# Performance work log

Hardware: AMD Instinct MI355X
Metric: run time of the kernel (lower is better)

## Reference

```python
import jax, jax.numpy as jnp
import numpy as np
from jax import lax

B, T, D = 2048, 300, 40
H = 64          # BasicLSTMCell num_units
D1 = 128        # dense1 units
OUT = 512       # out_dim (num speakers)
FORGET_BIAS = 1.0
BN_EPS = 1e-3   # tf.layers.BatchNormalization default


def setup_inputs() -> dict:
    key = jax.random.key(0)
    ks = jax.random.split(key, 10)
    X = jax.random.normal(ks[0], (B, T, D), dtype=jnp.float32)
    seq_length = jax.random.randint(ks[1], (B,), 1, T + 1).astype(jnp.int32)
    # BasicLSTMCell kernel: [input_dim + H, 4H], gate order i, j, f, o
    lstm_kernel = jax.random.normal(ks[2], (D + H, 4 * H), dtype=jnp.float32) * 0.08
    lstm_bias = jnp.zeros((4 * H,), dtype=jnp.float32)
    W1 = jax.random.normal(ks[3], (H, D1), dtype=jnp.float32) * 0.1
    b1 = jnp.zeros((D1,), dtype=jnp.float32)
    gamma = jnp.ones((D1,), dtype=jnp.float32)
    beta = jnp.zeros((D1,), dtype=jnp.float32)
    moving_mean = jnp.zeros((D1,), dtype=jnp.float32)
    moving_var = jnp.ones((D1,), dtype=jnp.float32)
    W2 = jax.random.normal(ks[4], (D1, OUT), dtype=jnp.float32) * 0.1
    b2 = jnp.zeros((OUT,), dtype=jnp.float32)
    return {"X": X, "seq_length": seq_length,
            "lstm_kernel": lstm_kernel, "lstm_bias": lstm_bias,
            "W1": W1, "b1": b1, "gamma": gamma, "beta": beta,
            "moving_mean": moving_mean, "moving_var": moving_var,
            "W2": W2, "b2": b2}


def reference(X, seq_length, lstm_kernel, lstm_bias, W1, b1, gamma, beta,
              moving_mean, moving_var, W2, b2):
    b = X.shape[0]
    c0 = jnp.zeros((b, H), dtype=X.dtype)
    h0 = jnp.zeros((b, H), dtype=X.dtype)

    def step(carry, x_t):
        c, h = carry
        z = jnp.concatenate([x_t, h], axis=1) @ lstm_kernel + lstm_bias
        i, j, f, o = jnp.split(z, 4, axis=1)
        new_c = c * jax.nn.sigmoid(f + FORGET_BIAS) + jax.nn.sigmoid(i) * jnp.tanh(j)
        new_h = jnp.tanh(new_c) * jax.nn.sigmoid(o)
        return (new_c, new_h), new_h

    _, outs = lax.scan(step, (c0, h0), jnp.swapaxes(X, 0, 1))  # [T, B, H]
    outs = jnp.swapaxes(outs, 0, 1)  # [B, T, H]

    # gather last valid timestep per sample
    idx = (seq_length - 1).astype(jnp.int32)
    final = jnp.take_along_axis(outs, idx[:, None, None], axis=1)[:, 0, :]  # [B, H]

    x = jax.nn.relu(final @ W1 + b1)
    # BatchNorm in inference mode (training=False): use moving statistics
    x = gamma * (x - moving_mean) * lax.rsqrt(moving_var + BN_EPS) + beta
    return jax.nn.softmax(x @ W2 + b2, axis=-1)
```

## Files before the change

kernel.cpp:

```cpp
#include <hip/hip_runtime.h>
#include <stdint.h>

#define TT 300
#define DD 40
#define SB 8
#define AROWH 192
#define ABYTES (16 * AROWH * 2)
#define WROW 224

typedef __attribute__((ext_vector_type(8))) short short8;
typedef __attribute__((ext_vector_type(4))) float f32x4;

__device__ __forceinline__ ushort f2bf(float f) {
  uint32_t b = __float_as_uint(f);
  b += 0x7FFFu + ((b >> 16) & 1u);
  return (ushort)(b >> 16);
}

__device__ __forceinline__ void bar() {
  asm volatile("s_waitcnt lgkmcnt(0)" ::: "memory");
  __builtin_amdgcn_s_barrier();
  asm volatile("" ::: "memory");
}

__device__ __forceinline__ int aswz(int row, int colh) {
  return ((row * AROWH + colh) * 2) ^ ((row & 7) << 4);
}

__global__ __launch_bounds__(512, 2) void lstm_mfma_kernel(
    const float* __restrict__ X, const int* __restrict__ seqlen,
    const float* __restrict__ Wk, const float* __restrict__ bias,
    float* __restrict__ hfin)
{
  __shared__ ushort shmem[64 * WROW];
  char* const Ab = reinterpret_cast<char*>(shmem);

  const int tid = threadIdx.x;
  const int wv = tid >> 6, lane = tid & 63;
  const int q = lane >> 4, n = lane & 15, m = n & 7, b = n >> 3;
  const int s0 = blockIdx.x * SB;

  short8 Bf[6][2];
  for (int c = 0; c < 4; ++c) {
    for (int i = tid; i < 64 * 192; i += 512) {
      int cc = i & 63, kp = i >> 6;
      int nb = cc & 15, nt = (cc >> 4) & 1, ws = cc >> 5;
      int g = nt + 2 * (nb >> 3);
      int uu = (2 * c + ws) * 8 + (nb & 7);
      int col = g * 64 + uu;
      ushort v = 0;
      if (kp < 40) {
        v = f2bf(Wk[kp * 256 + col]);
      } else if (kp < 42) {
        float bv = bias[col] + ((g == 2) ? 1.0f : 0.0f);
        ushort hi = f2bf(bv);
        v = (kp == 40) ? hi : f2bf(bv - __uint_as_float((uint32_t)hi << 16));
      } else if (kp >= 64) {
        v = f2bf(Wk[(40 + ((kp - 64) >> 1)) * 256 + col]);
      }
      shmem[cc * WROW + kp] = v;
    }
    __syncthreads();
    if ((wv >> 1) == c) {
      const int cbase = (wv & 1) * 32;
      #pragma unroll
      for (int kt = 0; kt < 6; ++kt) {
        #pragma unroll
        for (int nt = 0; nt < 2; ++nt)
          Bf[kt][nt] = *reinterpret_cast<const short8*>(
              &shmem[(cbase + nt * 16 + n) * WROW + kt * 32 + q * 8]);
      }
    }
    __syncthreads();
  }

  for (int i = tid; i < 6144; i += 512) shmem[i] = 0;
  __syncthreads();

  const int u = wv * 8 + m;
  const int sl = 2 * q + b;
  const int len = seqlen[s0 + sl];
  int ml = seqlen[s0 + (lane & 7)];
  #pragma unroll
  for (int off = 1; off < 8; off <<= 1) ml = max(ml, __shfl_xor(ml, off));

  const bool hasX = (tid < SB * DD);
  const int sA = (tid * 205) >> 13, dA = tid - sA * 40;
  const int rA = 4 * (sA >> 1) + (sA & 1);
  const float* pA = X + (size_t)(s0 + sA) * (TT * DD) + dA;
  const int xb = aswz(rA, dA);

  if (tid < 16) {
    int s = tid & 7, bb = tid >> 3;
    int row = 4 * (s >> 1) + (s & 1);
    *reinterpret_cast<uint32_t*>(Ab + bb * ABYTES + aswz(row, 40)) = 0x3F803F80u;
  }
  float xv = 0.f;
  if (hasX) {
    *reinterpret_cast<ushort*>(Ab + xb) = f2bf(pA[0]);
    if (ml > 1) xv = pA[DD];
  }
  __syncthreads();
  pA += 2 * DD;

  int aoff[6];
  #pragma unroll
  for (int kt = 0; kt < 6; ++kt)
    aoff[kt] = (n * 384 + kt * 64 + q * 16) ^ (m << 4);

  float cst = 0.f, hf = 0.f;
  int rb = 0, wb = ABYTES;
  const int hb = aswz(4 * q + b, 64 + 2 * u);

  for (int t = 0; t < ml; ++t) {
    short8 Ax0 = *reinterpret_cast<const short8*>(Ab + rb + aoff[0]);
    short8 Ax1 = *reinterpret_cast<const short8*>(Ab + rb + aoff[1]);
    short8 Ah[4];
    #pragma unroll
    for (int k2 = 0; k2 < 4; ++k2)
      Ah[k2] = *reinterpret_cast<const short8*>(Ab + rb + aoff[k2 + 2]);

    f32x4 zero4 = {0.f, 0.f, 0.f, 0.f};
    f32x4 ac0[2], ac1[2], ac2[2], ac3[2];
    #pragma unroll
    for (int nt = 0; nt < 2; ++nt) {
      ac0[nt] = __builtin_amdgcn_mfma_f32_16x16x32_bf16(Ax0, Bf[0][nt], zero4, 0, 0, 0);
      ac0[nt] = __builtin_amdgcn_mfma_f32_16x16x32_bf16(Ax1, Bf[1][nt], ac0[nt], 0, 0, 0);
    }

    if (hasX && t + 1 < ml) *reinterpret_cast<ushort*>(Ab + wb + xb) = f2bf(xv);
    float xn = 0.f;
    if (hasX && t + 2 < ml) { xn = pA[0]; pA += DD; }

    #pragma unroll
    for (int nt = 0; nt < 2; ++nt) {
      ac1[nt] = __builtin_amdgcn_mfma_f32_16x16x32_bf16(Ah[0], Bf[2][nt], zero4, 0, 0, 0);
      ac2[nt] = __builtin_amdgcn_mfma_f32_16x16x32_bf16(Ah[1], Bf[3][nt], zero4, 0, 0, 0);
      ac3[nt] = __builtin_amdgcn_mfma_f32_16x16x32_bf16(Ah[2], Bf[4][nt], zero4, 0, 0, 0);
      ac0[nt] = __builtin_amdgcn_mfma_f32_16x16x32_bf16(Ah[3], Bf[5][nt], ac0[nt], 0, 0, 0);
    }
    f32x4 z0 = (ac0[0] + ac1[0]) + (ac2[0] + ac3[0]);
    f32x4 z1 = (ac0[1] + ac1[1]) + (ac2[1] + ac3[1]);

    float p00 = __shfl_xor(z0[0], 8);
    float p01 = __shfl_xor(z0[1], 8);
    float p10 = __shfl_xor(z1[0], 8);
    float p11 = __shfl_xor(z1[1], 8);
    float gi = b ? p01 : z0[0];
    float gf = b ? z0[1] : p00;
    float gj = b ? p11 : z1[0];
    float go = b ? z1[1] : p10;

    float Ef = __expf(-gf), Ei = __expf(-gi), Ej = __expf(2.f * gj);
    float nc = fmaf(cst, __builtin_amdgcn_rcpf(1.f + Ef),
                    (Ej - 1.f) * __builtin_amdgcn_rcpf((1.f + Ei) * (1.f + Ej)));
    float En = __expf(2.f * fminf(nc, 44.f)), Eo = __expf(-go);
    float nh = (En - 1.f) * __builtin_amdgcn_rcpf((1.f + En) * (1.f + Eo));
    cst = nc;
    if (t == len - 1) hf = nh;

    ushort hh = (ushort)(__float_as_uint(nh) >> 16);
    float rem = nh - __uint_as_float((uint32_t)hh << 16);
    ushort hl = (ushort)(__float_as_uint(rem) >> 16);
    *reinterpret_cast<uint32_t*>(Ab + wb + hb) = (uint32_t)hh | ((uint32_t)hl << 16);

    bar();
    rb ^= ABYTES; wb ^= ABYTES;
    xv = xn;
  }

  hfin[(size_t)(s0 + sl) * 64 + u] = hf;
}

__global__ __launch_bounds__(256, 1) void head_kernel(
    const float* __restrict__ hfin,
    const float* __restrict__ W1, const float* __restrict__ b1,
    const float* __restrict__ gamma, const float* __restrict__ beta,
    const float* __restrict__ mmean, const float* __restrict__ mvar,
    const float* __restrict__ W2, const float* __restrict__ b2,
    float* __restrict__ out)
{
  __shared__ float hl[16 * 64];
  __shared__ float d1t[128 * 20];
  __shared__ float lg[16 * 516];
  const int tid = threadIdx.x;
  const int b0 = blockIdx.x * 16;

  for (int i = tid; i < 16 * 64; i += 256) hl[i] = hfin[(size_t)b0 * 64 + i];
  __syncthreads();

  {
    const int j = tid & 127, sg = tid >> 7;
    float acc[8];
    const float bb = b1[j];
    #pragma unroll
    for (int s = 0; s < 8; ++s) acc[s] = bb;
    for (int k = 0; k < 64; ++k) {
      float w = W1[k * 128 + j];
      #pragma unroll
      for (int s = 0; s < 8; ++s) acc[s] = fmaf(hl[(sg * 8 + s) * 64 + k], w, acc[s]);
    }
    const float ga = gamma[j], be = beta[j], mm = mmean[j];
    const float iv = rsqrtf(mvar[j] + 1e-3f);
    #pragma unroll
    for (int s = 0; s < 8; ++s) {
      float v = fmaxf(acc[s], 0.f);
      d1t[j * 20 + sg * 8 + s] = ga * (v - mm) * iv + be;
    }
  }
  __syncthreads();

  {
    const int cA = tid * 2;
    float accA[16], accB[16];
    const float bA = b2[cA], bB = b2[cA + 1];
    #pragma unroll
    for (int s = 0; s < 16; ++s) { accA[s] = bA; accB[s] = bB; }
    for (int k = 0; k < 128; ++k) {
      const float2 w = *reinterpret_cast<const float2*>(&W2[k * 512 + cA]);
      const f32x4 dq0 = *reinterpret_cast<const f32x4*>(&d1t[k * 20]);
      const f32x4 dq1 = *reinterpret_cast<const f32x4*>(&d1t[k * 20 + 4]);
      const f32x4 dq2 = *reinterpret_cast<const f32x4*>(&d1t[k * 20 + 8]);
      const f32x4 dq3 = *reinterpret_cast<const f32x4*>(&d1t[k * 20 + 12]);
      #pragma unroll
      for (int s = 0; s < 4; ++s) {
        accA[s]      = fmaf(dq0[s], w.x, accA[s]);      accB[s]      = fmaf(dq0[s], w.y, accB[s]);
        accA[s + 4]  = fmaf(dq1[s], w.x, accA[s + 4]);  accB[s + 4]  = fmaf(dq1[s], w.y, accB[s + 4]);
        accA[s + 8]  = fmaf(dq2[s], w.x, accA[s + 8]);  accB[s + 8]  = fmaf(dq2[s], w.y, accB[s + 8]);
        accA[s + 12] = fmaf(dq3[s], w.x, accA[s + 12]); accB[s + 12] = fmaf(dq3[s], w.y, accB[s + 12]);
      }
    }
    #pragma unroll
    for (int s = 0; s < 16; ++s) {
      lg[s * 516 + cA]     = accA[s];
      lg[s * 516 + cA + 1] = accB[s];
    }
  }
  __syncthreads();

  {
    const int w = tid >> 6, lane = tid & 63;
    #pragma unroll
    for (int si = 0; si < 4; ++si) {
      const int s = w * 4 + si;
      float v[8];
      float mx = -3.4e38f;
      #pragma unroll
      for (int i = 0; i < 8; ++i) { v[i] = lg[s * 516 + lane + 64 * i]; mx = fmaxf(mx, v[i]); }
      #pragma unroll
      for (int off = 1; off < 64; off <<= 1) mx = fmaxf(mx, __shfl_xor(mx, off));
      float sum = 0.f;
      #pragma unroll
      for (int i = 0; i < 8; ++i) { v[i] = __expf(v[i] - mx); sum += v[i]; }
      #pragma unroll
      for (int off = 1; off < 64; off <<= 1) sum += __shfl_xor(sum, off);
      const float inv = __builtin_amdgcn_rcpf(sum);
      #pragma unroll
      for (int i = 0; i < 8; ++i)
        out[(size_t)(b0 + s) * 512 + lane + 64 * i] = v[i] * inv;
    }
  }
}

extern "C" void kernel_launch(void* const* d_in, const int* in_sizes, int n_in,
                              void* d_out, int out_size, void* d_ws, size_t ws_size,
                              hipStream_t stream) {
  const float* X      = (const float*)d_in[0];
  const int*   seqlen = (const int*)d_in[1];
  const float* Wk     = (const float*)d_in[2];
  const float* bias   = (const float*)d_in[3];
  const float* W1     = (const float*)d_in[4];
  const float* b1     = (const float*)d_in[5];
  const float* gam    = (const float*)d_in[6];
  const float* bet    = (const float*)d_in[7];
  const float* mmean  = (const float*)d_in[8];
  const float* mvar   = (const float*)d_in[9];
  const float* W2     = (const float*)d_in[10];
  const float* b2     = (const float*)d_in[11];
  float* out  = (float*)d_out;
  float* hfin = (float*)d_ws;

  lstm_mfma_kernel<<<dim3(2048 / SB), dim3(512), 0, stream>>>(X, seqlen, Wk, bias, hfin);
  head_kernel<<<dim3(128), dim3(256), 0, stream>>>(hfin, W1, b1, gam, bet,
                                                   mmean, mvar, W2, b2, out);
}
```

Baseline: 363.5 us.

## Compact A tile to 8 rows, single accumulator chain, unroll double buffer

Result: faster. 350.7 us (-3.5%).

```diff
diff --git a/kernel.cpp b/kernel.cpp
--- a/kernel.cpp
+++ b/kernel.cpp
@@ -4,8 +4,7 @@
 #define TT 300
 #define DD 40
 #define SB 8
-#define AROWH 192
-#define ABYTES (16 * AROWH * 2)
+#define ABYTES (8 * 192 * 2)
 #define WROW 224
 
 typedef __attribute__((ext_vector_type(8))) short short8;
@@ -24,7 +23,7 @@
 }
 
 __device__ __forceinline__ int aswz(int row, int colh) {
-  return ((row * AROWH + colh) * 2) ^ ((row & 7) << 4);
+  return ((row * 192 + colh) * 2) ^ (row << 4);
 }
 
 __global__ __launch_bounds__(512, 2) void lstm_mfma_kernel(
@@ -74,11 +73,12 @@
     __syncthreads();
   }
 
-  for (int i = tid; i < 6144; i += 512) shmem[i] = 0;
-  __syncthreads();
-
+  for (int i = tid; i < 3072; i += 512) shmem[i] = 0;
+  __syncthreads();
+
+  const int hi2 = q >> 1;
   const int u = wv * 8 + m;
-  const int sl = 2 * q + b;
+  const int sl = (q & 1) * 4 + hi2 * 2 + b;
   const int len = seqlen[s0 + sl];
   int ml = seqlen[s0 + (lane & 7)];
   #pragma unroll
@@ -86,14 +86,12 @@
 
   const bool hasX = (tid < SB * DD);
   const int sA = (tid * 205) >> 13, dA = tid - sA * 40;
-  const int rA = 4 * (sA >> 1) + (sA & 1);
   const float* pA = X + (size_t)(s0 + sA) * (TT * DD) + dA;
-  const int xb = aswz(rA, dA);
+  const int xb = aswz(sA, dA);
 
   if (tid < 16) {
     int s = tid & 7, bb = tid >> 3;
-    int row = 4 * (s >> 1) + (s & 1);
-    *reinterpret_cast<uint32_t*>(Ab + bb * ABYTES + aswz(row, 40)) = 0x3F803F80u;
+    *reinterpret_cast<uint32_t*>(Ab + bb * ABYTES + aswz(s, 40)) = 0x3F803F80u;
   }
   float xv = 0.f;
   if (hasX) {
@@ -106,50 +104,53 @@
   int aoff[6];
   #pragma unroll
   for (int kt = 0; kt < 6; ++kt)
-    aoff[kt] = (n * 384 + kt * 64 + q * 16) ^ (m << 4);
+    aoff[kt] = (m * 384 + kt * 64 + q * 16) ^ (m << 4);
 
   float cst = 0.f, hf = 0.f;
-  int rb = 0, wb = ABYTES;
-  const int hb = aswz(4 * q + b, 64 + 2 * u);
-
-  for (int t = 0; t < ml; ++t) {
-    short8 Ax0 = *reinterpret_cast<const short8*>(Ab + rb + aoff[0]);
-    short8 Ax1 = *reinterpret_cast<const short8*>(Ab + rb + aoff[1]);
-    short8 Ah[4];
-    #pragma unroll
-    for (int k2 = 0; k2 < 4; ++k2)
-      Ah[k2] = *reinterpret_cast<const short8*>(Ab + rb + aoff[k2 + 2]);
-
-    f32x4 zero4 = {0.f, 0.f, 0.f, 0.f};
-    f32x4 ac0[2], ac1[2], ac2[2], ac3[2];
-    #pragma unroll
-    for (int nt = 0; nt < 2; ++nt) {
-      ac0[nt] = __builtin_amdgcn_mfma_f32_16x16x32_bf16(Ax0, Bf[0][nt], zero4, 0, 0, 0);
-      ac0[nt] = __builtin_amdgcn_mfma_f32_16x16x32_bf16(Ax1, Bf[1][nt], ac0[nt], 0, 0, 0);
-    }
-
-    if (hasX && t + 1 < ml) *reinterpret_cast<ushort*>(Ab + wb + xb) = f2bf(xv);
+  float xvl = xv;
+  const int hb = aswz(sl, 64 + 2 * u);
+  const f32x4 zero4 = {0.f, 0.f, 0.f, 0.f};
+
+  auto STEP = [&](int t, int RB, int WB) {
+    short8 Ax0 = *reinterpret_cast<const short8*>(Ab + RB + aoff[0]);
+    short8 Ax1 = *reinterpret_cast<const short8*>(Ab + RB + aoff[1]);
+    short8 Ah0 = *reinterpret_cast<const short8*>(Ab + RB + aoff[2]);
+    short8 Ah1 = *reinterpret_cast<const short8*>(Ab + RB + aoff[3]);
+    short8 Ah2 = *reinterpret_cast<const short8*>(Ab + RB + aoff[4]);
+    short8 Ah3 = *reinterpret_cast<const short8*>(Ab + RB + aoff[5]);
+
+    f32x4 ac0 = __builtin_amdgcn_mfma_f32_16x16x32_bf16(Ax0, Bf[0][0], zero4, 0, 0, 0);
+    f32x4 ac1 = __builtin_amdgcn_mfma_f32_16x16x32_bf16(Ax0, Bf[0][1], zero4, 0, 0, 0);
+    ac0 = __builtin_amdgcn_mfma_f32_16x16x32_bf16(Ax1, Bf[1][0], ac0, 0, 0, 0);
+    ac1 = __builtin_amdgcn_mfma_f32_16x16x32_bf16(Ax1, Bf[1][1], ac1, 0, 0, 0);
+
+    if (hasX && t + 1 < ml) *reinterpret_cast<ushort*>(Ab + WB + xb) = f2bf(xvl);
     float xn = 0.f;
     if (hasX && t + 2 < ml) { xn = pA[0]; pA += DD; }
 
-    #pragma unroll
-    for (int nt = 0; nt < 2; ++nt) {
-      ac1[nt] = __builtin_amdgcn_mfma_f32_16x16x32_bf16(Ah[0], Bf[2][nt], zero4, 0, 0, 0);
-      ac2[nt] = __builtin_amdgcn_mfma_f32_16x16x32_bf16(Ah[1], Bf[3][nt], zero4, 0, 0, 0);
-      ac3[nt] = __builtin_amdgcn_mfma_f32_16x16x32_bf16(Ah[2], Bf[4][nt], zero4, 0, 0, 0);
-      ac0[nt] = __builtin_amdgcn_mfma_f32_16x16x32_bf16(Ah[3], Bf[5][nt], ac0[nt], 0, 0, 0);
-    }
-    f32x4 z0 = (ac0[0] + ac1[0]) + (ac2[0] + ac3[0]);
-    f32x4 z1 = (ac0[1] + ac1[1]) + (ac2[1] + ac3[1]);
-
-    float p00 = __shfl_xor(z0[0], 8);
-    float p01 = __shfl_xor(z0[1], 8);
-    float p10 = __shfl_xor(z1[0], 8);
-    float p11 = __shfl_xor(z1[1], 8);
-    float gi = b ? p01 : z0[0];
-    float gf = b ? z0[1] : p00;
-    float gj = b ? p11 : z1[0];
-    float go = b ? z1[1] : p10;
+    ac0 = __builtin_amdgcn_mfma_f32_16x16x32_bf16(Ah0, Bf[2][0], ac0, 0, 0, 0);
+    ac1 = __builtin_amdgcn_mfma_f32_16x16x32_bf16(Ah0, Bf[2][1], ac1, 0, 0, 0);
+    ac0 = __builtin_amdgcn_mfma_f32_16x16x32_bf16(Ah1, Bf[3][0], ac0, 0, 0, 0);
+    ac1 = __builtin_amdgcn_mfma_f32_16x16x32_bf16(Ah1, Bf[3][1], ac1, 0, 0, 0);
+    ac0 = __builtin_amdgcn_mfma_f32_16x16x32_bf16(Ah2, Bf[4][0], ac0, 0, 0, 0);
+    ac1 = __builtin_amdgcn_mfma_f32_16x16x32_bf16(Ah2, Bf[4][1], ac1, 0, 0, 0);
+    ac0 = __builtin_amdgcn_mfma_f32_16x16x32_bf16(Ah3, Bf[5][0], ac0, 0, 0, 0);
+    ac1 = __builtin_amdgcn_mfma_f32_16x16x32_bf16(Ah3, Bf[5][1], ac1, 0, 0, 0);
+
+    float v0_s0 = hi2 ? ac0[2] : ac0[0];
+    float v0_s1 = hi2 ? ac0[3] : ac0[1];
+    float v1_s0 = hi2 ? ac1[2] : ac1[0];
+    float v1_s1 = hi2 ? ac1[3] : ac1[1];
+    float own0 = b ? v0_s1 : v0_s0;
+    float own1 = b ? v1_s1 : v1_s0;
+    float snd0 = b ? v0_s0 : v0_s1;
+    float snd1 = b ? v1_s0 : v1_s1;
+    float rcv0 = __shfl_xor(snd0, 8);
+    float rcv1 = __shfl_xor(snd1, 8);
+    float gi = b ? rcv0 : own0;
+    float gj = b ? rcv1 : own1;
+    float gf = b ? own0 : rcv0;
+    float go = b ? own1 : rcv1;
 
     float Ef = __expf(-gf), Ei = __expf(-gi), Ej = __expf(2.f * gj);
     float nc = fmaf(cst, __builtin_amdgcn_rcpf(1.f + Ef),
@@ -162,11 +163,16 @@
     ushort hh = (ushort)(__float_as_uint(nh) >> 16);
     float rem = nh - __uint_as_float((uint32_t)hh << 16);
     ushort hl = (ushort)(__float_as_uint(rem) >> 16);
-    *reinterpret_cast<uint32_t*>(Ab + wb + hb) = (uint32_t)hh | ((uint32_t)hl << 16);
+    *reinterpret_cast<uint32_t*>(Ab + WB + hb) = (uint32_t)hh | ((uint32_t)hl << 16);
 
     bar();
-    rb ^= ABYTES; wb ^= ABYTES;
-    xv = xn;
+    xvl = xn;
+  };
+
+  for (int t = 0; t < ml; ) {
+    STEP(t, 0, ABYTES); ++t;
+    if (t >= ml) break;
+    STEP(t, ABYTES, 0); ++t;
   }
 
   hfin[(size_t)(s0 + sl) * 64 + u] = hf;
```
